# Kernel tuning notes

Hardware: AMD Instinct MI355X
Metric: run time of the kernel (lower is better)

The kernel has to match this reference:

```python
import jax, jax.numpy as jnp
import numpy as np
from jax import lax

N, H, W = 16, 112, 112
CIN, COUT, K = 256, 256, 3
STRIDE, PAD = 1, 1


def setup_inputs() -> dict:
    key = jax.random.key(0)
    kx, kw = jax.random.split(key)
    # int8-valued activations and weights, stored as int32 for portable integer conv
    x = jax.random.randint(kx, (N, H, W, CIN), -128, 128, dtype=jnp.int32)
    # weight layout matches the torch module: (out_channels, kH, kW, in_channels) == OHWI
    weight = jax.random.randint(kw, (COUT, K, K, CIN), -128, 128, dtype=jnp.int32)
    return {"x": x, "weight": weight}


def reference(x, weight):
    y = lax.conv_general_dilated(
        x,
        weight,
        window_strides=(STRIDE, STRIDE),
        padding=[(PAD, PAD), (PAD, PAD)],
        dimension_numbers=("NHWC", "OHWI", "NHWC"),
        preferred_element_type=jnp.int32,
    )
    return y  # (N, H, W, COUT) int32
```

## Files before the change

### kernel.cpp

```cpp
#include <hip/hip_runtime.h>
#include <stdint.h>

#define NN   16
#define HH   112
#define WW   112
#define CIN  256
#define COUT 256
#define HP   114
#define WP   114
#define M_TOTAL (NN * HH * WW)
#define XP_BYTES ((size_t)NN * HP * WP * CIN)
#define WPK_BYTES ((size_t)9 * COUT * CIN)

typedef int v4i __attribute__((ext_vector_type(4)));

__device__ __forceinline__ void load_lds16(const void* g, void* l) {
  __builtin_amdgcn_global_load_lds(
      (const __attribute__((address_space(1))) void*)g,
      (__attribute__((address_space(3))) void*)l, 16, 0, 0);
}

__global__ void pack_x_kernel(const int* __restrict__ x, char* __restrict__ xp) {
  int t = blockIdx.x * 256 + threadIdx.x;
  int g = t & 15;
  int p = t >> 4;
  int w = p % WW;
  int t2 = p / WW;
  int h = t2 % HH;
  int n = t2 / HH;
  const int* src = x + (size_t)p * CIN + g * 16;
  int4 i0 = ((const int4*)src)[0];
  int4 i1 = ((const int4*)src)[1];
  int4 i2 = ((const int4*)src)[2];
  int4 i3 = ((const int4*)src)[3];
  int vals[16] = {i0.x, i0.y, i0.z, i0.w, i1.x, i1.y, i1.z, i1.w,
                  i2.x, i2.y, i2.z, i2.w, i3.x, i3.y, i3.z, i3.w};
  int4 ov;
  char* pc = (char*)&ov;
#pragma unroll
  for (int i = 0; i < 16; i++) pc[i] = (char)vals[i];
  size_t dst = (((size_t)n * HP + (h + 1)) * WP + (w + 1)) * CIN + (size_t)g * 16;
  *(int4*)(xp + dst) = ov;
}

__global__ void zero_border_kernel(char* __restrict__ xp) {
  int t = blockIdx.x * 256 + threadIdx.x;
  int g = t & 15;
  int pix = t >> 4;
  int n = pix / 452;
  int b = pix % 452;
  int h, w;
  if (b < 114) { h = 0; w = b; }
  else if (b < 228) { h = 113; w = b - 114; }
  else { int r = b - 228; h = 1 + (r >> 1); w = (r & 1) ? 113 : 0; }
  size_t dst = (((size_t)n * HP + h) * WP + w) * CIN + (size_t)g * 16;
  *(int4*)(xp + dst) = make_int4(0, 0, 0, 0);
}

__global__ void pack_w_kernel(const int* __restrict__ wgt, char* __restrict__ wp) {
  int t = blockIdx.x * 256 + threadIdx.x;
  int g = t & 15;
  int r = t >> 4;
  int tap = r % 9;
  int cout = r / 9;
  const int* src = wgt + ((size_t)(cout * 9 + tap)) * CIN + g * 16;
  int4 i0 = ((const int4*)src)[0];
  int4 i1 = ((const int4*)src)[1];
  int4 i2 = ((const int4*)src)[2];
  int4 i3 = ((const int4*)src)[3];
  int vals[16] = {i0.x, i0.y, i0.z, i0.w, i1.x, i1.y, i1.z, i1.w,
                  i2.x, i2.y, i2.z, i2.w, i3.x, i3.y, i3.z, i3.w};
  int4 ov;
  char* pc = (char*)&ov;
#pragma unroll
  for (int i = 0; i < 16; i++) pc[i] = (char)vals[i];
  size_t dst = ((size_t)tap * COUT + cout) * CIN + (size_t)g * 16;
  *(int4*)(wp + dst) = ov;
}

__global__ __launch_bounds__(256) void conv_mfma_kernel(const char* __restrict__ xp,
                                                        const char* __restrict__ wp,
                                                        int* __restrict__ out) {
  __shared__ __align__(16) char As[128 * 64];
  __shared__ __align__(16) char Bs[128 * 64];
  const int tid = threadIdx.x;
  const int lane = tid & 63;
  const int wave = tid >> 6;
  const int ntile = blockIdx.x & 1;
  const int mtile = blockIdx.x >> 1;

  const char* gA[2];
  const char* gB[2];
  char* lA[2];
  char* lB[2];
#pragma unroll
  for (int j = 0; j < 2; j++) {
    int c = wave * 2 + j;
    int row = c * 16 + (lane >> 2);
    int colg = (lane & 3) ^ ((row >> 1) & 3);
    int m = mtile * 128 + row;
    int w = m % WW;
    int t2 = m / WW;
    int h = t2 % HH;
    int n = t2 / HH;
    gA[j] = xp + (((size_t)n * HP + h) * WP + w) * CIN + (size_t)colg * 16;
    lA[j] = As + c * 1024;
    int co = ntile * 128 + row;
    gB[j] = wp + (size_t)co * CIN + (size_t)colg * 16;
    lB[j] = Bs + c * 1024;
  }

  const int wm = wave & 1;
  const int wn = wave >> 1;
  int aoff[4], boff[4];
#pragma unroll
  for (int i = 0; i < 4; i++) {
    int ra = wm * 64 + i * 16 + (lane & 15);
    aoff[i] = ra * 64 + (((lane >> 4) ^ ((ra >> 1) & 3)) * 16);
    int rb = wn * 64 + i * 16 + (lane & 15);
    boff[i] = rb * 64 + (((lane >> 4) ^ ((rb >> 1) & 3)) * 16);
  }

  v4i acc[4][4];
#pragma unroll
  for (int i = 0; i < 4; i++)
#pragma unroll
    for (int j = 0; j < 4; j++) acc[i][j] = (v4i){0, 0, 0, 0};

#pragma unroll 1
  for (int ks = 0; ks < 36; ks++) {
    const int tap = ks >> 2;
    const int kb = ks & 3;
    const int ky = tap / 3;
    const int kx = tap - ky * 3;
    const int offA = (ky * WP + kx) * CIN + kb * 64;
    const int offB = tap * (COUT * CIN) + kb * 64;
    __syncthreads();
    load_lds16(gA[0] + offA, lA[0]);
    load_lds16(gA[1] + offA, lA[1]);
    load_lds16(gB[0] + offB, lB[0]);
    load_lds16(gB[1] + offB, lB[1]);
    __syncthreads();
    v4i af[4], bf[4];
#pragma unroll
    for (int i = 0; i < 4; i++) af[i] = *(const v4i*)(As + aoff[i]);
#pragma unroll
    for (int i = 0; i < 4; i++) bf[i] = *(const v4i*)(Bs + boff[i]);
#pragma unroll
    for (int i = 0; i < 4; i++)
#pragma unroll
      for (int j = 0; j < 4; j++)
        acc[i][j] = __builtin_amdgcn_mfma_i32_16x16x64_i8(af[i], bf[j], acc[i][j], 0, 0, 0);
  }

#pragma unroll
  for (int i = 0; i < 4; i++) {
    const int mg = mtile * 128 + wm * 64 + i * 16 + ((lane >> 4) * 4);
#pragma unroll
    for (int r = 0; r < 4; r++) {
      int* orow = out + (size_t)(mg + r) * COUT + ntile * 128 + wn * 64 + (lane & 15);
#pragma unroll
      for (int j = 0; j < 4; j++) orow[j * 16] = acc[i][j][r];
    }
  }
}

__global__ void conv_naive_kernel(const int* __restrict__ x, const int* __restrict__ wgt,
                                  int* __restrict__ out, int total) {
  int idx = blockIdx.x * 256 + threadIdx.x;
  if (idx >= total) return;
  int co = idx & 255;
  int p = idx >> 8;
  int w = p % WW;
  int t2 = p / WW;
  int h = t2 % HH;
  int n = t2 / HH;
  int acc = 0;
  for (int ky = 0; ky < 3; ky++) {
    int ih = h + ky - 1;
    if (ih < 0 || ih >= HH) continue;
    for (int kx = 0; kx < 3; kx++) {
      int iw = w + kx - 1;
      if (iw < 0 || iw >= WW) continue;
      const int* xs = x + (((size_t)n * HH + ih) * WW + iw) * CIN;
      const int* ws = wgt + ((size_t)co * 9 + ky * 3 + kx) * CIN;
      for (int ci = 0; ci < CIN; ci++) acc += xs[ci] * ws[ci];
    }
  }
  out[idx] = acc;
}

extern "C" void kernel_launch(void* const* d_in, const int* in_sizes, int n_in,
                              void* d_out, int out_size, void* d_ws, size_t ws_size,
                              hipStream_t stream) {
  const int* x = (const int*)d_in[0];
  const int* wgt = (const int*)d_in[1];
  int* out = (int*)d_out;
  const size_t need = XP_BYTES + WPK_BYTES;
  if (ws_size >= need) {
    char* xp = (char*)d_ws;
    char* wp = xp + XP_BYTES;
    pack_x_kernel<<<(M_TOTAL * 16) / 256, 256, 0, stream>>>(x, xp);
    zero_border_kernel<<<(7232 * 16) / 256, 256, 0, stream>>>(xp);
    pack_w_kernel<<<(2304 * 16) / 256, 256, 0, stream>>>(wgt, wp);
    conv_mfma_kernel<<<(M_TOTAL / 128) * 2, 256, 0, stream>>>(xp, wp, out);
  } else {
    conv_naive_kernel<<<(out_size + 255) / 256, 256, 0, stream>>>(x, wgt, out, out_size);
  }
}
```

Measured before the change: 504.1 us.

## Widen conv tile to full COUT per block and vectorize int8 packing

The MFMA conv block now computes all 256 output channels for its 128 pixels instead of splitting COUT across two blocks. The A tile is loaded once rather than twice, and each wave issues 32 MFMAs per k-step instead of 16. This doubles the accumulator registers to 128 per lane, so launch bounds are set to 2 blocks, and the grid halves. The pack kernels also replace byte-wise char stores with shift/mask packing into int4.

```diff
diff --git a/kernel.cpp b/kernel.cpp
--- a/kernel.cpp
+++ b/kernel.cpp
@@ -18,6 +18,10 @@
   __builtin_amdgcn_global_load_lds(
       (const __attribute__((address_space(1))) void*)g,
       (__attribute__((address_space(3))) void*)l, 16, 0, 0);
+}
+
+__device__ __forceinline__ int pack4(int a, int b, int c, int d) {
+  return (a & 255) | ((b & 255) << 8) | ((c & 255) << 16) | (d << 24);
 }
 
 __global__ void pack_x_kernel(const int* __restrict__ x, char* __restrict__ xp) {
@@ -33,12 +37,10 @@
   int4 i1 = ((const int4*)src)[1];
   int4 i2 = ((const int4*)src)[2];
   int4 i3 = ((const int4*)src)[3];
-  int vals[16] = {i0.x, i0.y, i0.z, i0.w, i1.x, i1.y, i1.z, i1.w,
-                  i2.x, i2.y, i2.z, i2.w, i3.x, i3.y, i3.z, i3.w};
-  int4 ov;
-  char* pc = (char*)&ov;
-#pragma unroll
-  for (int i = 0; i < 16; i++) pc[i] = (char)vals[i];
+  int4 ov = make_int4(pack4(i0.x, i0.y, i0.z, i0.w),
+                      pack4(i1.x, i1.y, i1.z, i1.w),
+                      pack4(i2.x, i2.y, i2.z, i2.w),
+                      pack4(i3.x, i3.y, i3.z, i3.w));
   size_t dst = (((size_t)n * HP + (h + 1)) * WP + (w + 1)) * CIN + (size_t)g * 16;
   *(int4*)(xp + dst) = ov;
 }
@@ -68,64 +70,70 @@
   int4 i1 = ((const int4*)src)[1];
   int4 i2 = ((const int4*)src)[2];
   int4 i3 = ((const int4*)src)[3];
-  int vals[16] = {i0.x, i0.y, i0.z, i0.w, i1.x, i1.y, i1.z, i1.w,
-                  i2.x, i2.y, i2.z, i2.w, i3.x, i3.y, i3.z, i3.w};
-  int4 ov;
-  char* pc = (char*)&ov;
-#pragma unroll
-  for (int i = 0; i < 16; i++) pc[i] = (char)vals[i];
+  int4 ov = make_int4(pack4(i0.x, i0.y, i0.z, i0.w),
+                      pack4(i1.x, i1.y, i1.z, i1.w),
+                      pack4(i2.x, i2.y, i2.z, i2.w),
+                      pack4(i3.x, i3.y, i3.z, i3.w));
   size_t dst = ((size_t)tap * COUT + cout) * CIN + (size_t)g * 16;
   *(int4*)(wp + dst) = ov;
 }
 
-__global__ __launch_bounds__(256) void conv_mfma_kernel(const char* __restrict__ xp,
-                                                        const char* __restrict__ wp,
-                                                        int* __restrict__ out) {
+__global__ __launch_bounds__(256, 2) void conv_mfma_kernel(const char* __restrict__ xp,
+                                                           const char* __restrict__ wp,
+                                                           int* __restrict__ out) {
   __shared__ __align__(16) char As[128 * 64];
-  __shared__ __align__(16) char Bs[128 * 64];
+  __shared__ __align__(16) char Bs[256 * 64];
   const int tid = threadIdx.x;
   const int lane = tid & 63;
   const int wave = tid >> 6;
-  const int ntile = blockIdx.x & 1;
-  const int mtile = blockIdx.x >> 1;
-
-  const char* gA[2];
-  const char* gB[2];
-  char* lA[2];
-  char* lB[2];
-#pragma unroll
-  for (int j = 0; j < 2; j++) {
-    int c = wave * 2 + j;
-    int row = c * 16 + (lane >> 2);
-    int colg = (lane & 3) ^ ((row >> 1) & 3);
-    int m = mtile * 128 + row;
-    int w = m % WW;
-    int t2 = m / WW;
-    int h = t2 % HH;
-    int n = t2 / HH;
-    gA[j] = xp + (((size_t)n * HP + h) * WP + w) * CIN + (size_t)colg * 16;
-    lA[j] = As + c * 1024;
-    int co = ntile * 128 + row;
-    gB[j] = wp + (size_t)co * CIN + (size_t)colg * 16;
-    lB[j] = Bs + c * 1024;
+  const int mtile = blockIdx.x;
+
+  const char* gptr[6];
+  char* lptr[6];
+  int  isA[6];
+#pragma unroll
+  for (int j = 0; j < 6; j++) {
+    int c = wave * 6 + j;
+    if (c < 8) {
+      int row = c * 16 + (lane >> 2);
+      int colg = (lane & 3) ^ ((row >> 1) & 3);
+      int m = mtile * 128 + row;
+      int w = m % WW;
+      int t2 = m / WW;
+      int h = t2 % HH;
+      int n = t2 / HH;
+      gptr[j] = xp + (((size_t)n * HP + h) * WP + w) * CIN + (size_t)colg * 16;
+      lptr[j] = As + c * 1024;
+      isA[j] = 1;
+    } else {
+      int cb = c - 8;
+      int row = cb * 16 + (lane >> 2);
+      int colg = (lane & 3) ^ ((row >> 1) & 3);
+      gptr[j] = wp + (size_t)row * CIN + (size_t)colg * 16;
+      lptr[j] = Bs + cb * 1024;
+      isA[j] = 0;
+    }
   }
 
   const int wm = wave & 1;
   const int wn = wave >> 1;
-  int aoff[4], boff[4];
+  int aoff[4], boff[8];
 #pragma unroll
   for (int i = 0; i < 4; i++) {
     int ra = wm * 64 + i * 16 + (lane & 15);
     aoff[i] = ra * 64 + (((lane >> 4) ^ ((ra >> 1) & 3)) * 16);
-    int rb = wn * 64 + i * 16 + (lane & 15);
-    boff[i] = rb * 64 + (((lane >> 4) ^ ((rb >> 1) & 3)) * 16);
-  }
-
-  v4i acc[4][4];
+  }
+#pragma unroll
+  for (int j = 0; j < 8; j++) {
+    int rb = wn * 128 + j * 16 + (lane & 15);
+    boff[j] = rb * 64 + (((lane >> 4) ^ ((rb >> 1) & 3)) * 16);
+  }
+
+  v4i acc[4][8];
 #pragma unroll
   for (int i = 0; i < 4; i++)
 #pragma unroll
-    for (int j = 0; j < 4; j++) acc[i][j] = (v4i){0, 0, 0, 0};
+    for (int j = 0; j < 8; j++) acc[i][j] = (v4i){0, 0, 0, 0};
 
 #pragma unroll 1
   for (int ks = 0; ks < 36; ks++) {
@@ -136,20 +144,19 @@
     const int offA = (ky * WP + kx) * CIN + kb * 64;
     const int offB = tap * (COUT * CIN) + kb * 64;
     __syncthreads();
-    load_lds16(gA[0] + offA, lA[0]);
-    load_lds16(gA[1] + offA, lA[1]);
-    load_lds16(gB[0] + offB, lB[0]);
-    load_lds16(gB[1] + offB, lB[1]);
+#pragma unroll
+    for (int j = 0; j < 6; j++)
+      load_lds16(gptr[j] + (isA[j] ? offA : offB), lptr[j]);
     __syncthreads();
-    v4i af[4], bf[4];
+    v4i af[4], bf[8];
 #pragma unroll
     for (int i = 0; i < 4; i++) af[i] = *(const v4i*)(As + aoff[i]);
 #pragma unroll
-    for (int i = 0; i < 4; i++) bf[i] = *(const v4i*)(Bs + boff[i]);
+    for (int j = 0; j < 8; j++) bf[j] = *(const v4i*)(Bs + boff[j]);
 #pragma unroll
     for (int i = 0; i < 4; i++)
 #pragma unroll
-      for (int j = 0; j < 4; j++)
+      for (int j = 0; j < 8; j++)
         acc[i][j] = __builtin_amdgcn_mfma_i32_16x16x64_i8(af[i], bf[j], acc[i][j], 0, 0, 0);
   }
 
@@ -158,9 +165,9 @@
     const int mg = mtile * 128 + wm * 64 + i * 16 + ((lane >> 4) * 4);
 #pragma unroll
     for (int r = 0; r < 4; r++) {
-      int* orow = out + (size_t)(mg + r) * COUT + ntile * 128 + wn * 64 + (lane & 15);
-#pragma unroll
-      for (int j = 0; j < 4; j++) orow[j * 16] = acc[i][j][r];
+      int* orow = out + (size_t)(mg + r) * COUT + wn * 128 + (lane & 15);
+#pragma unroll
+      for (int j = 0; j < 8; j++) orow[j * 16] = acc[i][j][r];
     }
   }
 }
@@ -203,7 +210,7 @@
     pack_x_kernel<<<(M_TOTAL * 16) / 256, 256, 0, stream>>>(x, xp);
     zero_border_kernel<<<(7232 * 16) / 256, 256, 0, stream>>>(xp);
     pack_w_kernel<<<(2304 * 16) / 256, 256, 0, stream>>>(wgt, wp);
-    conv_mfma_kernel<<<(M_TOTAL / 128) * 2, 256, 0, stream>>>(xp, wp, out);
+    conv_mfma_kernel<<<M_TOTAL / 128, 256, 0, stream>>>(xp, wp, out);
   } else {
     conv_naive_kernel<<<(out_size + 255) / 256, 256, 0, stream>>>(x, wgt, out, out_size);
   }
```

New measurement: 481.4 us. -4.5%, faster.
